# Kernel tuning notes

Measured on AMD Instinct MI355X. Metric: run time of the kernel, lower is better.

The kernel has to match this reference:

```python
import jax, jax.numpy as jnp
import numpy as np

NUM_HEADS = 12
DIM = 768


def setup_inputs() -> dict:
    key = jax.random.key(0)
    ks = jax.random.split(key, 7)
    B, S, E = 8, 1024, DIM
    s = 0.02
    return {
        "x": jax.random.normal(ks[0], (B, S, E), dtype=jnp.float32),
        "Wq": jax.random.normal(ks[1], (E, E), dtype=jnp.float32) * s,
        "bq": jnp.zeros((E,), dtype=jnp.float32),
        "Wk": jax.random.normal(ks[2], (E, E), dtype=jnp.float32) * s,
        "bk": jnp.zeros((E,), dtype=jnp.float32),
        "Wo": jax.random.normal(ks[3], (E, E), dtype=jnp.float32) * s,
        "bo": jnp.zeros((E,), dtype=jnp.float32),
    }


def reference(x, Wq, bq, Wk, bk, Wo, bo):
    B, S, E = x.shape
    n = NUM_HEADS
    d = E // n
    scale = d ** (-0.5)

    def heads(t):  # [B,S,E] -> [B,n,S,d]
        return t.reshape(B, S, n, d).transpose(0, 2, 1, 3)

    q = heads(x @ Wq.T + bq)
    k = heads(x @ Wk.T + bk)
    v = k  # faithful to source bug: v = self.k_w(x)

    attn = jnp.einsum('bnqd,bnkd->bnqk', q, k) * scale  # [B,n,S,S]
    attn = jax.nn.softmax(attn, axis=-1)
    out = jnp.einsum('bnqk,bnkd->bnqd', attn, v)  # [B,n,S,d]
    out = out.transpose(0, 2, 1, 3).reshape(B, S, E)
    return out @ Wo.T + bo
```

## Files before the change

kernel.cpp:

```cpp
#include <hip/hip_runtime.h>
#include <stdint.h>


using short8   = __attribute__((ext_vector_type(8))) short;
using float4v  = __attribute__((ext_vector_type(4))) float;
using float16v = __attribute__((ext_vector_type(16))) float;

struct __align__(8) U2 { unsigned x, y; };

__device__ __forceinline__ void async16(void* lds, const void* g) {
  __builtin_amdgcn_global_load_lds(
      (const __attribute__((address_space(1))) void*)g,
      (__attribute__((address_space(3))) void*)lds, 16, 0, 0);
}

__device__ __forceinline__ unsigned bf16b(float f) {
  union { float f; unsigned u; } v; v.f = f;
  unsigned r = v.u + 0x7FFFu + ((v.u >> 16) & 1u);
  return r >> 16;
}

__global__ __launch_bounds__(256) void cvt_bf16(const float* __restrict__ in,
                                                unsigned short* __restrict__ out,
                                                int n8) {
  int i = blockIdx.x * 256 + threadIdx.x;
  if (i >= n8) return;
  const float4v* p = (const float4v*)in;
  float4v a = p[i * 2], b = p[i * 2 + 1];
  short8 o;
  o[0] = (short)bf16b(a[0]); o[1] = (short)bf16b(a[1]);
  o[2] = (short)bf16b(a[2]); o[3] = (short)bf16b(a[3]);
  o[4] = (short)bf16b(b[0]); o[5] = (short)bf16b(b[1]);
  o[6] = (short)bf16b(b[2]); o[7] = (short)bf16b(b[3]);
  ((short8*)out)[i] = o;
}

template <int MODE>
__global__ __launch_bounds__(256) void gemm_bt(
    const unsigned short* __restrict__ A, const unsigned short* __restrict__ B,
    const int M, const int N, const int K,
    const float* __restrict__ bias0, const float* __restrict__ bias1,
    void* __restrict__ outa, void* __restrict__ outb, void* __restrict__ outc) {
  __shared__ __align__(16) unsigned short a_l[4096];
  __shared__ __align__(16) unsigned short b_l[4096];
  const int tid = threadIdx.x;
  const int w = tid >> 6, lane = tid & 63;
  const int Q4 = lane >> 4, r = lane & 15;
  const int m0 = blockIdx.y * 128;
  const int n0 = blockIdx.x * 128;
  const int wm = w >> 1, wn = w & 1;

  float4v acc[4][4];
#pragma unroll
  for (int i = 0; i < 4; ++i)
#pragma unroll
    for (int j = 0; j < 4; ++j)
#pragma unroll
      for (int g = 0; g < 4; ++g) acc[i][j][g] = 0.0f;

  const unsigned short* Ab = A + (size_t)m0 * K;
  const unsigned short* Bb = B + (size_t)n0 * K;

  for (int kt = 0; kt < K; kt += 32) {
    __syncthreads();
#pragma unroll
    for (int ci = 0; ci < 2; ++ci) {
      int c = w * 2 + ci;
      int row = c * 16 + r;
      async16(&a_l[c * 512 + lane * 8], Ab + (size_t)row * K + kt + Q4 * 8);
      async16(&b_l[c * 512 + lane * 8], Bb + (size_t)row * K + kt + Q4 * 8);
    }
    __syncthreads();

    short8 af[4], bf[4];
#pragma unroll
    for (int i = 0; i < 4; ++i) {
      af[i] = *(const short8*)&a_l[(wm * 4 + i) * 512 + lane * 8];
      bf[i] = *(const short8*)&b_l[(wn * 4 + i) * 512 + lane * 8];
    }
#pragma unroll
    for (int mt = 0; mt < 4; ++mt)
#pragma unroll
      for (int nt = 0; nt < 4; ++nt)
        acc[mt][nt] = __builtin_amdgcn_mfma_f32_16x16x32_bf16(
            af[mt], bf[nt], acc[mt][nt], 0, 0, 0);
  }

  if (MODE == 0) {
    const bool isq = (n0 < 768);
    const float* bias = isq ? bias0 : bias1;
    unsigned short* outp = (unsigned short*)(isq ? outa : outb);
    const int nb = isq ? n0 : (n0 - 768);
    const float scl = isq ? 0.125f : 1.0f;
#pragma unroll
    for (int nt = 0; nt < 4; ++nt) {
      int n = nb + wn * 64 + nt * 16 + r;
      float bv = bias[n];
#pragma unroll
      for (int mt = 0; mt < 4; ++mt) {
        int m = m0 + wm * 64 + mt * 16 + Q4 * 4;
#pragma unroll
        for (int g = 0; g < 4; ++g)
          outp[(size_t)(m + g) * 768 + n] = (unsigned short)bf16b((acc[mt][nt][g] + bv) * scl);
      }
    }
    if (!isq) {
      unsigned short* ktp = (unsigned short*)outc;
      const int bq = m0 >> 10;
      const int sbase = (m0 & 1023) + wm * 64 + (Q4 & 1) * 8 + (Q4 >> 1) * 4;
#pragma unroll
      for (int nt = 0; nt < 4; ++nt) {
        int n = nb + wn * 64 + nt * 16 + r;
        int hh = n >> 6, dd = n & 63;
        float bv = bias[n];
#pragma unroll
        for (int mt = 0; mt < 4; ++mt) {
          int ns = sbase + mt * 16;
          unsigned lo = bf16b(acc[mt][nt][0] + bv) | (bf16b(acc[mt][nt][1] + bv) << 16);
          unsigned hi = bf16b(acc[mt][nt][2] + bv) | (bf16b(acc[mt][nt][3] + bv) << 16);
          *(U2*)(ktp + (size_t)((bq * 12 + hh) * 64 + dd) * 1024 + ns) = U2{lo, hi};
        }
      }
    }
  } else {
    float* outp = (float*)outa;
#pragma unroll
    for (int nt = 0; nt < 4; ++nt) {
      int n = n0 + wn * 64 + nt * 16 + r;
      float bv = bias0[n];
#pragma unroll
      for (int mt = 0; mt < 4; ++mt) {
        int m = m0 + wm * 64 + mt * 16 + Q4 * 4;
#pragma unroll
        for (int g = 0; g < 4; ++g)
          outp[(size_t)(m + g) * (size_t)N + n] = acc[mt][nt][g] + bv;
      }
    }
  }
}

__global__ __launch_bounds__(256, 3) void attn_fused(
    const unsigned short* __restrict__ qg,
    const unsigned short* __restrict__ kg,
    const unsigned short* __restrict__ ktg,
    unsigned short* __restrict__ ao) {
  __shared__ __align__(16) unsigned short q_l[8192];
  __shared__ __align__(16) unsigned short k_l[8192];
  __shared__ __align__(16) unsigned short vt_l[8192];

  const int tid = threadIdx.x;
  const int w = tid >> 6, lane = tid & 63;
  const int l31 = lane & 31, hi = lane >> 5;
  const int bid = blockIdx.x;
  const int b = bid & 7;
  const int h = bid >> 6;
  const int qt = (bid >> 3) & 7;
  const int q0 = qt * 128;
  const int bh = b * 12 + h;

#pragma unroll
  for (int ci = 0; ci < 4; ++ci) {
    int c = w * 4 + ci;
    async16(&q_l[c * 512 + lane * 8],
            qg + ((size_t)(b * 1024 + q0 + (c >> 2) * 32 + l31) * 768 + h * 64 + (c & 3) * 16 + hi * 8));
    async16(&k_l[c * 512 + lane * 8],
            kg + ((size_t)(b * 1024 + (c >> 2) * 32 + l31) * 768 + h * 64 + (c & 3) * 16 + hi * 8));
    async16(&vt_l[c * 512 + lane * 8],
            ktg + ((size_t)(bh * 64 + (c >> 3) * 32 + l31) * 1024 + (c & 7) * 16 + hi * 8));
  }
  __syncthreads();

  short8 bfq[4];
#pragma unroll
  for (int kb = 0; kb < 4; ++kb)
    bfq[kb] = *(const short8*)&q_l[(w * 4 + kb) * 512 + lane * 8];

  float16v o_acc[2];
#pragma unroll
  for (int db = 0; db < 2; ++db)
#pragma unroll
    for (int e = 0; e < 16; ++e) o_acc[db][e] = 0.0f;
  float ps = 0.0f;

#pragma unroll 1
  for (int it = 0; it < 8; ++it) {
    if (it > 0) {
      const int s0 = it * 128;
      __syncthreads();
#pragma unroll
      for (int ci = 0; ci < 4; ++ci) {
        int c = w * 4 + ci;
        async16(&k_l[c * 512 + lane * 8],
                kg + ((size_t)(b * 1024 + s0 + (c >> 2) * 32 + l31) * 768 + h * 64 + (c & 3) * 16 + hi * 8));
        async16(&vt_l[c * 512 + lane * 8],
                ktg + ((size_t)(bh * 64 + (c >> 3) * 32 + l31) * 1024 + s0 + (c & 7) * 16 + hi * 8));
      }
      __syncthreads();
    }

    float16v sc[4];
#pragma unroll
    for (int sb = 0; sb < 4; ++sb)
#pragma unroll
      for (int e = 0; e < 16; ++e) sc[sb][e] = 0.0f;
#pragma unroll
    for (int sb = 0; sb < 4; ++sb)
#pragma unroll
      for (int kb = 0; kb < 4; ++kb) {
        short8 af = *(const short8*)&k_l[(sb * 4 + kb) * 512 + lane * 8];
        sc[sb] = __builtin_amdgcn_mfma_f32_32x32x16_bf16(af, bfq[kb], sc[sb], 0, 0, 0);
      }

#pragma unroll
    for (int sb = 0; sb < 4; ++sb) {
      float pe[16];
#pragma unroll
      for (int e = 0; e < 16; ++e) pe[e] = __expf(sc[sb][e]);
#pragma unroll
      for (int e = 0; e < 16; ++e) ps += pe[e];
      short8 pf0, pf1;
#pragma unroll
      for (int e = 0; e < 8; ++e) {
        pf0[e] = (short)bf16b(pe[e]);
        pf1[e] = (short)bf16b(pe[8 + e]);
      }
#pragma unroll
      for (int db = 0; db < 2; ++db) {
        short8 vf0 = *(const short8*)&vt_l[(db * 8 + sb * 2) * 512 + lane * 8];
        o_acc[db] = __builtin_amdgcn_mfma_f32_32x32x16_bf16(vf0, pf0, o_acc[db], 0, 0, 0);
        short8 vf1 = *(const short8*)&vt_l[(db * 8 + sb * 2 + 1) * 512 + lane * 8];
        o_acc[db] = __builtin_amdgcn_mfma_f32_32x32x16_bf16(vf1, pf1, o_acc[db], 0, 0, 0);
      }
    }
  }

  ps += __shfl_xor(ps, 32, 64);
  const float inv = 1.0f / ps;
  const size_t rowbase = (size_t)(b * 1024 + q0 + w * 32 + l31) * 768 + h * 64;
#pragma unroll
  for (int db = 0; db < 2; ++db)
#pragma unroll
    for (int qq = 0; qq < 4; ++qq) {
      float v0 = o_acc[db][qq * 4 + 0] * inv;
      float v1 = o_acc[db][qq * 4 + 1] * inv;
      float v2 = o_acc[db][qq * 4 + 2] * inv;
      float v3 = o_acc[db][qq * 4 + 3] * inv;
      unsigned lo = bf16b(v0) | (bf16b(v1) << 16);
      unsigned hh = bf16b(v2) | (bf16b(v3) << 16);
      *(U2*)(ao + rowbase + db * 32 + qq * 8 + hi * 4) = U2{lo, hh};
    }
}

extern "C" void kernel_launch(void* const* d_in, const int* in_sizes, int n_in,
                              void* d_out, int out_size, void* d_ws, size_t ws_size,
                              hipStream_t stream) {
  const float* x  = (const float*)d_in[0];
  const float* Wq = (const float*)d_in[1];
  const float* bq = (const float*)d_in[2];
  const float* Wk = (const float*)d_in[3];
  const float* bk = (const float*)d_in[4];
  const float* Wo = (const float*)d_in[5];
  const float* bo = (const float*)d_in[6];
  (void)in_sizes; (void)n_in; (void)out_size; (void)ws_size;

  char* ws = (char*)d_ws;
  unsigned short* x_b   = (unsigned short*)(ws);
  unsigned short* wqk_b = (unsigned short*)(ws + 12582912);
  unsigned short* wo_b  = (unsigned short*)(ws + 14942208);
  unsigned short* q_b   = (unsigned short*)(ws + 16121856);
  unsigned short* k_b   = (unsigned short*)(ws + 28704768);
  unsigned short* kt_b  = (unsigned short*)(ws + 41287680);
  unsigned short* ao_b  = (unsigned short*)(ws + 53870592);

  cvt_bf16<<<3072, 256, 0, stream>>>(x, x_b, 786432);
  cvt_bf16<<<288, 256, 0, stream>>>(Wq, wqk_b, 73728);
  cvt_bf16<<<288, 256, 0, stream>>>(Wk, wqk_b + 589824, 73728);
  cvt_bf16<<<288, 256, 0, stream>>>(Wo, wo_b, 73728);

  gemm_bt<0><<<dim3(12, 64), 256, 0, stream>>>(x_b, wqk_b, 8192, 1536, 768,
                                               bq, bk, q_b, k_b, kt_b);
  attn_fused<<<768, 256, 0, stream>>>(q_b, k_b, kt_b, ao_b);
  gemm_bt<1><<<dim3(6, 64), 256, 0, stream>>>(ao_b, wo_b, 8192, 768, 768,
                                              bo, nullptr, d_out, nullptr, nullptr);
}
```

Measured before the change: 221.0 us.

## Rewrite projection GEMMs as single-wave triple-buffered kernels and merge weight casts

Replaces the 256-thread, sync-per-k-step GEMM with a one-wavefront kernel that computes a 128x64 tile. It triple-buffers the async global-to-LDS loads and waits on vmcnt counters instead of workgroup barriers, so loads overlap the MFMA work and barrier stalls go away. K is hardcoded to 768. The three weight conversion launches are merged into one kernel. The cost is that each wave issues more loads and holds more accumulator registers, with only one wave per block, which could lower occupancy and latency hiding.

```diff
diff --git a/kernel.cpp b/kernel.cpp
--- a/kernel.cpp
+++ b/kernel.cpp
@@ -13,6 +13,8 @@
       (const __attribute__((address_space(1))) void*)g,
       (__attribute__((address_space(3))) void*)lds, 16, 0, 0);
 }
+
+#define VM_WAIT(n) asm volatile("s_waitcnt vmcnt(" #n ")" ::: "memory")
 
 __device__ __forceinline__ unsigned bf16b(float f) {
   union { float f; unsigned u; } v; v.f = f;
@@ -35,56 +37,88 @@
   ((short8*)out)[i] = o;
 }
 
+__global__ __launch_bounds__(256) void cvt_w3(const float* __restrict__ w0,
+                                              const float* __restrict__ w1,
+                                              const float* __restrict__ w2,
+                                              unsigned short* __restrict__ o0,
+                                              unsigned short* __restrict__ o1,
+                                              unsigned short* __restrict__ o2) {
+  int mi = blockIdx.x / 288;
+  int i = (blockIdx.x - mi * 288) * 256 + threadIdx.x;
+  const float* in = (mi == 0) ? w0 : (mi == 1) ? w1 : w2;
+  unsigned short* out = (mi == 0) ? o0 : (mi == 1) ? o1 : o2;
+  const float4v* p = (const float4v*)in;
+  float4v a = p[i * 2], b = p[i * 2 + 1];
+  short8 o;
+  o[0] = (short)bf16b(a[0]); o[1] = (short)bf16b(a[1]);
+  o[2] = (short)bf16b(a[2]); o[3] = (short)bf16b(a[3]);
+  o[4] = (short)bf16b(b[0]); o[5] = (short)bf16b(b[1]);
+  o[6] = (short)bf16b(b[2]); o[7] = (short)bf16b(b[3]);
+  ((short8*)out)[i] = o;
+}
+
 template <int MODE>
-__global__ __launch_bounds__(256) void gemm_bt(
+__global__ __launch_bounds__(64, 1) void sgemm(
     const unsigned short* __restrict__ A, const unsigned short* __restrict__ B,
-    const int M, const int N, const int K,
     const float* __restrict__ bias0, const float* __restrict__ bias1,
     void* __restrict__ outa, void* __restrict__ outb, void* __restrict__ outc) {
-  __shared__ __align__(16) unsigned short a_l[4096];
-  __shared__ __align__(16) unsigned short b_l[4096];
-  const int tid = threadIdx.x;
-  const int w = tid >> 6, lane = tid & 63;
-  const int Q4 = lane >> 4, r = lane & 15;
+  __shared__ __align__(16) unsigned short aL[3][4096];
+  __shared__ __align__(16) unsigned short bL[3][2048];
+  const int lane = threadIdx.x;
+  const int r = lane & 15, Q4 = lane >> 4;
+  const int n0 = blockIdx.x * 64;
   const int m0 = blockIdx.y * 128;
-  const int n0 = blockIdx.x * 128;
-  const int wm = w >> 1, wn = w & 1;
-
-  float4v acc[4][4];
-#pragma unroll
-  for (int i = 0; i < 4; ++i)
+
+  const unsigned short* Ab = A + (size_t)(m0 + r) * 768 + Q4 * 8;
+  const unsigned short* Bb = B + (size_t)(n0 + r) * 768 + Q4 * 8;
+
+  auto stage = [&](int bi, int kk) {
+#pragma unroll
+    for (int c = 0; c < 8; ++c)
+      async16(&aL[bi][c * 512 + lane * 8], Ab + c * 16 * 768 + kk);
+#pragma unroll
+    for (int c = 0; c < 4; ++c)
+      async16(&bL[bi][c * 512 + lane * 8], Bb + c * 16 * 768 + kk);
+  };
+
+  short8 fa[8], fb[4];
+  auto loadf = [&](int bi) {
+#pragma unroll
+    for (int i = 0; i < 8; ++i) fa[i] = *(const short8*)&aL[bi][i * 512 + lane * 8];
+#pragma unroll
+    for (int i = 0; i < 4; ++i) fb[i] = *(const short8*)&bL[bi][i * 512 + lane * 8];
+  };
+
+  float4v acc[8][4];
+#pragma unroll
+  for (int i = 0; i < 8; ++i)
 #pragma unroll
     for (int j = 0; j < 4; ++j)
 #pragma unroll
       for (int g = 0; g < 4; ++g) acc[i][j][g] = 0.0f;
 
-  const unsigned short* Ab = A + (size_t)m0 * K;
-  const unsigned short* Bb = B + (size_t)n0 * K;
-
-  for (int kt = 0; kt < K; kt += 32) {
-    __syncthreads();
-#pragma unroll
-    for (int ci = 0; ci < 2; ++ci) {
-      int c = w * 2 + ci;
-      int row = c * 16 + r;
-      async16(&a_l[c * 512 + lane * 8], Ab + (size_t)row * K + kt + Q4 * 8);
-      async16(&b_l[c * 512 + lane * 8], Bb + (size_t)row * K + kt + Q4 * 8);
-    }
-    __syncthreads();
-
-    short8 af[4], bf[4];
-#pragma unroll
-    for (int i = 0; i < 4; ++i) {
-      af[i] = *(const short8*)&a_l[(wm * 4 + i) * 512 + lane * 8];
-      bf[i] = *(const short8*)&b_l[(wn * 4 + i) * 512 + lane * 8];
-    }
-#pragma unroll
-    for (int mt = 0; mt < 4; ++mt)
+  auto dot = [&]() {
+#pragma unroll
+    for (int mt = 0; mt < 8; ++mt)
 #pragma unroll
       for (int nt = 0; nt < 4; ++nt)
         acc[mt][nt] = __builtin_amdgcn_mfma_f32_16x16x32_bf16(
-            af[mt], bf[nt], acc[mt][nt], 0, 0, 0);
+            fa[mt], fb[nt], acc[mt][nt], 0, 0, 0);
+  };
+
+  stage(0, 0); stage(1, 32);
+  VM_WAIT(12); loadf(0);
+  stage(2, 64); dot(); VM_WAIT(12); loadf(1);
+#pragma unroll 1
+  for (int j = 0; j < 7; ++j) {
+    const int kb = j * 96;
+    stage(0, kb + 96);  dot(); VM_WAIT(12); loadf(2);
+    stage(1, kb + 128); dot(); VM_WAIT(12); loadf(0);
+    stage(2, kb + 160); dot(); VM_WAIT(12); loadf(1);
   }
+  dot();
+  VM_WAIT(0); loadf(2);
+  dot();
 
   if (MODE == 0) {
     const bool isq = (n0 < 768);
@@ -94,11 +128,11 @@
     const float scl = isq ? 0.125f : 1.0f;
 #pragma unroll
     for (int nt = 0; nt < 4; ++nt) {
-      int n = nb + wn * 64 + nt * 16 + r;
+      int n = nb + nt * 16 + r;
       float bv = bias[n];
 #pragma unroll
-      for (int mt = 0; mt < 4; ++mt) {
-        int m = m0 + wm * 64 + mt * 16 + Q4 * 4;
+      for (int mt = 0; mt < 8; ++mt) {
+        int m = m0 + mt * 16 + Q4 * 4;
 #pragma unroll
         for (int g = 0; g < 4; ++g)
           outp[(size_t)(m + g) * 768 + n] = (unsigned short)bf16b((acc[mt][nt][g] + bv) * scl);
@@ -107,14 +141,14 @@
     if (!isq) {
       unsigned short* ktp = (unsigned short*)outc;
       const int bq = m0 >> 10;
-      const int sbase = (m0 & 1023) + wm * 64 + (Q4 & 1) * 8 + (Q4 >> 1) * 4;
+      const int sbase = (m0 & 1023) + (Q4 & 1) * 8 + (Q4 >> 1) * 4;
 #pragma unroll
       for (int nt = 0; nt < 4; ++nt) {
-        int n = nb + wn * 64 + nt * 16 + r;
+        int n = nb + nt * 16 + r;
         int hh = n >> 6, dd = n & 63;
         float bv = bias[n];
 #pragma unroll
-        for (int mt = 0; mt < 4; ++mt) {
+        for (int mt = 0; mt < 8; ++mt) {
           int ns = sbase + mt * 16;
           unsigned lo = bf16b(acc[mt][nt][0] + bv) | (bf16b(acc[mt][nt][1] + bv) << 16);
           unsigned hi = bf16b(acc[mt][nt][2] + bv) | (bf16b(acc[mt][nt][3] + bv) << 16);
@@ -126,14 +160,14 @@
     float* outp = (float*)outa;
 #pragma unroll
     for (int nt = 0; nt < 4; ++nt) {
-      int n = n0 + wn * 64 + nt * 16 + r;
+      int n = n0 + nt * 16 + r;
       float bv = bias0[n];
 #pragma unroll
-      for (int mt = 0; mt < 4; ++mt) {
-        int m = m0 + wm * 64 + mt * 16 + Q4 * 4;
+      for (int mt = 0; mt < 8; ++mt) {
+        int m = m0 + mt * 16 + Q4 * 4;
 #pragma unroll
         for (int g = 0; g < 4; ++g)
-          outp[(size_t)(m + g) * (size_t)N + n] = acc[mt][nt][g] + bv;
+          outp[(size_t)(m + g) * 768 + n] = acc[mt][nt][g] + bv;
       }
     }
   }
@@ -273,13 +307,9 @@
   unsigned short* ao_b  = (unsigned short*)(ws + 53870592);
 
   cvt_bf16<<<3072, 256, 0, stream>>>(x, x_b, 786432);
-  cvt_bf16<<<288, 256, 0, stream>>>(Wq, wqk_b, 73728);
-  cvt_bf16<<<288, 256, 0, stream>>>(Wk, wqk_b + 589824, 73728);
-  cvt_bf16<<<288, 256, 0, stream>>>(Wo, wo_b, 73728);
-
-  gemm_bt<0><<<dim3(12, 64), 256, 0, stream>>>(x_b, wqk_b, 8192, 1536, 768,
-                                               bq, bk, q_b, k_b, kt_b);
+  cvt_w3<<<864, 256, 0, stream>>>(Wq, Wk, Wo, wqk_b, wqk_b + 589824, wo_b);
+
+  sgemm<0><<<dim3(24, 64), 64, 0, stream>>>(x_b, wqk_b, bq, bk, q_b, k_b, kt_b);
   attn_fused<<<768, 256, 0, stream>>>(q_b, k_b, kt_b, ao_b);
-  gemm_bt<1><<<dim3(6, 64), 256, 0, stream>>>(ao_b, wo_b, 8192, 768, 768,
-                                              bo, nullptr, d_out, nullptr, nullptr);
-}
+  sgemm<1><<<dim3(12, 64), 64, 0, stream>>>(ao_b, wo_b, bo, nullptr, d_out, nullptr, nullptr);
+}
```

Result: slower. 232.8 us (+5.4%).
